# Performance work log

Measured on AMD Instinct MI355X. Metric: run time of the kernel, lower is better.

Reference implementation:

```python
import jax, jax.numpy as jnp
import numpy as np

C = 64
D = C // 8  # Q/K channel dim
B, H, W = 4, 64, 64


def setup_inputs() -> dict:
    key = jax.random.key(0)
    ks = jax.random.split(key, 4)
    x = jax.random.normal(ks[0], (B, C, H, W), dtype=jnp.float32)
    # 1x1 conv weights collapse to matrices [out_ch, in_ch]
    Wq = jax.random.normal(ks[1], (D, C), dtype=jnp.float32) * (1.0 / np.sqrt(C))
    Wk = jax.random.normal(ks[2], (D, C), dtype=jnp.float32) * (1.0 / np.sqrt(C))
    Wv = jax.random.normal(ks[3], (C, C), dtype=jnp.float32) * (1.0 / np.sqrt(C))
    bq = jnp.zeros((D,), jnp.float32)
    bk = jnp.zeros((D,), jnp.float32)
    bv = jnp.zeros((C,), jnp.float32)
    gamma = jnp.zeros((1,), jnp.float32)  # initialized to zero as in the module
    return {"x": x, "Wq": Wq, "bq": bq, "Wk": Wk, "bk": bk,
            "Wv": Wv, "bv": bv, "gamma": gamma}


def reference(x, Wq, bq, Wk, bk, Wv, bv, gamma):
    b, c, h, w = x.shape
    n = h * w
    xf = x.reshape(b, c, n)  # [B, C, N]
    # 1x1 convs == per-pixel linear projections
    q = jnp.einsum('dc,bcn->bdn', Wq, xf) + bq[None, :, None]  # [B, D, N]
    k = jnp.einsum('dc,bcn->bdn', Wk, xf) + bk[None, :, None]  # [B, D, N]
    v = jnp.einsum('ec,bcn->ben', Wv, xf) + bv[None, :, None]  # [B, C, N]
    # energy[b, i, j] = sum_d q[b, d, i] * k[b, d, j]  (query index i, key index j)
    energy = jnp.einsum('bdi,bdj->bij', q, k)  # [B, N, N]
    attn = jax.nn.softmax(energy, axis=-1)     # [B, N, N]
    # out[b, c, i] = sum_j v[b, c, j] * attn[b, i, j]
    out = jnp.einsum('bcj,bij->bci', v, attn)  # [B, C, N]
    out = out.reshape(b, c, h, w)
    return gamma[0] * out + x
```

## Files before the change

### kernel.cpp

```cpp
#include <hip/hip_runtime.h>
#include <hip/hip_bf16.h>

#define NPIX 4096

typedef __attribute__((ext_vector_type(16))) float f32x16;
typedef __attribute__((ext_vector_type(8))) short short8;

__device__ inline short f2bf(float f) {
  unsigned u = __float_as_uint(f);
  u += 0x7FFF + ((u >> 16) & 1);
  return (short)(u >> 16);
}

__device__ inline void gload16(const short* g, short* l) {
  __builtin_amdgcn_global_load_lds(
      (const __attribute__((address_space(1))) void*)g,
      (__attribute__((address_space(3))) void*)l, 16, 0, 0);
}

__global__ __launch_bounds__(256) void proj_kernel(
    const float* __restrict__ x,
    const float* __restrict__ Wq, const float* __restrict__ bq,
    const float* __restrict__ Wk, const float* __restrict__ bk,
    const float* __restrict__ Wv, const float* __restrict__ bv,
    short* __restrict__ Qp, short* __restrict__ Kp, short* __restrict__ Vi)
{
  const int job = blockIdx.x >> 6;
  const int p = (blockIdx.x & 63) * 256 + threadIdx.x;
  const int b = p >> 12, n = p & 4095;
  const float* xb = x + ((size_t)b << 18) + n;

  float xv[64];
#pragma unroll
  for (int c = 0; c < 64; ++c) xv[c] = xb[(size_t)c << 12];

  if (job < 2) {
    const float* W    = job ? Wk : Wq;
    const float* bias = job ? bk : bq;
    float a[8];
#pragma unroll
    for (int d = 0; d < 8; ++d) {
      float acc = bias[d];
#pragma unroll
      for (int c = 0; c < 64; ++c) acc = fmaf(W[d * 64 + c], xv[c], acc);
      a[d] = acc;
    }
    short8 o;
    if (job == 0) {
#pragma unroll
      for (int d = 0; d < 8; ++d) o[d] = f2bf(a[d] * 1.44269504f);
      *(short8*)(Qp + (size_t)p * 8) = o;
    } else {
#pragma unroll
      for (int d = 0; d < 8; ++d) o[d] = f2bf(a[d]);
      *(short8*)(Kp + (size_t)p * 8) = o;
    }
  } else {
    const int e0 = (job - 2) * 8;
    const size_t base = ((size_t)(b * 512 + (n >> 3)) * 64) * 8 + (n & 7);
#pragma unroll
    for (int i = 0; i < 8; ++i) {
      float acc = bv[e0 + i];
#pragma unroll
      for (int c = 0; c < 64; ++c) acc = fmaf(Wv[(e0 + i) * 64 + c], xv[c], acc);
      Vi[base + (size_t)(e0 + i) * 8] = f2bf(acc);
    }
  }
}

__device__ inline void pk_swap(const float* p, short8& A0, short8& A1) {
  unsigned u[8];
#pragma unroll
  for (int j = 0; j < 8; ++j)
    asm("v_cvt_pk_bf16_f32 %0, %1, %2" : "=v"(u[j]) : "v"(p[2 * j]), "v"(p[2 * j + 1]));
  asm("v_permlane32_swap_b32 %0, %1" : "+v"(u[0]), "+v"(u[2]));
  asm("v_permlane32_swap_b32 %0, %1" : "+v"(u[1]), "+v"(u[3]));
  asm("v_permlane32_swap_b32 %0, %1" : "+v"(u[4]), "+v"(u[6]));
  asm("v_permlane32_swap_b32 %0, %1" : "+v"(u[5]), "+v"(u[7]));
  union { unsigned w[4]; short8 s; } c0, c1;
  c0.w[0] = u[0]; c0.w[1] = u[1]; c0.w[2] = u[2]; c0.w[3] = u[3];
  c1.w[0] = u[4]; c1.w[1] = u[5]; c1.w[2] = u[6]; c1.w[3] = u[7];
  A0 = c0.s; A1 = c1.s;
}

__global__ __launch_bounds__(512, 2) void attn_kernel(
    const short* __restrict__ Qp, const short* __restrict__ Kp,
    const short* __restrict__ Vi,
    short* __restrict__ accB, float* __restrict__ psumW)
{
  __shared__ short kLds[2][1024];
  __shared__ short vLds[2][8192];

  const int tid  = threadIdx.x;
  const int wv   = tid >> 6;
  const int lane = tid & 63;
  const int lo   = lane & 31;
  const int hi   = lane >> 5;

  const int bid = blockIdx.x;
  const int ks  = bid & 3;
  const int qg  = (bid >> 2) & 15;
  const int b   = bid >> 6;
  const int Qgbase = (b << 12) + qg * 256 + wv * 32;

  short8 qf = {};
  if (hi == 0) qf = *(const short8*)(Qp + (size_t)(Qgbase + lo) * 8);

  const short* ksrc = Kp + ((size_t)(b << 12) + ks * 1024) * 8;
  const short* vsrc = Vi + (size_t)b * 262144 + (size_t)ks * 65536;

  auto stage = [&](int c, int buf) {
    const short* vs = vsrc + (size_t)c * 8192;
    gload16(vs + (size_t)tid * 8,         &vLds[buf][(tid & ~63) * 8]);
    gload16(vs + (size_t)(tid + 512) * 8, &vLds[buf][((tid + 512) & ~63) * 8]);
    if (tid < 128)
      gload16(ksrc + (size_t)c * 1024 + (size_t)tid * 8, &kLds[buf][(tid & ~63) * 8]);
  };

  f32x16 acc0 = {}, acc1 = {};
  float psum = 0.f;
  const f32x16 z = {};

  stage(0, 0);
  __syncthreads();

  for (int c = 0; c < 8; ++c) {
    if (c < 7) stage(c + 1, (c + 1) & 1);
    const int buf = c & 1;
#pragma unroll
    for (int i = 0; i < 4; ++i) {
      short8 kf = *(const short8*)&kLds[buf][(i * 32 + lo) * 8];
      f32x16 en = __builtin_amdgcn_mfma_f32_32x32x16_bf16(kf, qf, z, 0, 0, 0);
      float p[16];
#pragma unroll
      for (int j = 0; j < 16; ++j) p[j] = __builtin_amdgcn_exp2f(en[j]);
#pragma unroll
      for (int j = 0; j < 16; ++j) psum += p[j];
      short8 a0, a1;
      pk_swap(p, a0, a1);
      short8 v00 = *(const short8*)&vLds[buf][(i * 4 + hi) * 512 + lo * 8];
      short8 v01 = *(const short8*)&vLds[buf][(i * 4 + hi) * 512 + (32 + lo) * 8];
      short8 v10 = *(const short8*)&vLds[buf][(i * 4 + 2 + hi) * 512 + lo * 8];
      short8 v11 = *(const short8*)&vLds[buf][(i * 4 + 2 + hi) * 512 + (32 + lo) * 8];
      __builtin_amdgcn_s_setprio(1);
      acc0 = __builtin_amdgcn_mfma_f32_32x32x16_bf16(a0, v00, acc0, 0, 0, 0);
      acc1 = __builtin_amdgcn_mfma_f32_32x32x16_bf16(a0, v01, acc1, 0, 0, 0);
      acc0 = __builtin_amdgcn_mfma_f32_32x32x16_bf16(a1, v10, acc0, 0, 0, 0);
      acc1 = __builtin_amdgcn_mfma_f32_32x32x16_bf16(a1, v11, acc1, 0, 0, 0);
      __builtin_amdgcn_s_setprio(0);
    }
    __syncthreads();
  }

  float pfull = psum + __shfl_xor(psum, 32);
  if (hi == 0) psumW[ks * 16384 + Qgbase + lo] = pfull;

#pragma unroll
  for (int r = 0; r < 16; ++r) {
    const int q = (r & 3) + 8 * (r >> 2) + 4 * hi;
    const size_t base = ((size_t)(ks * 16384 + Qgbase + q)) << 6;
    accB[base + lo]      = f2bf(acc0[r]);
    accB[base + 32 + lo] = f2bf(acc1[r]);
  }
}

__global__ __launch_bounds__(256) void reduce_kernel(
    const short* __restrict__ accB, const float* __restrict__ psumW,
    const float* __restrict__ x, const float* __restrict__ gamma,
    float* __restrict__ out)
{
  __shared__ float accLds[64][65];
  __shared__ float sInv[64];

  const int tid = threadIdx.x;
  const int Qg0 = blockIdx.x * 64;
  const float g = gamma[0];

  if (tid < 64) {
    float s = 0.f;
#pragma unroll
    for (int ks = 0; ks < 4; ++ks) s += psumW[ks * 16384 + Qg0 + tid];
    sInv[tid] = g / s;
  }

  const int e2 = tid & 31;
  const int qr = tid >> 5;
#pragma unroll
  for (int qs = 0; qs < 8; ++qs) {
    const int qq = qr + qs * 8;
    float s0 = 0.f, s1 = 0.f;
#pragma unroll
    for (int ks = 0; ks < 4; ++ks) {
      const unsigned u = *(const unsigned*)&accB[(((size_t)(ks * 16384 + Qg0 + qq)) << 6) + e2 * 2];
      s0 += __uint_as_float(u << 16);
      s1 += __uint_as_float(u & 0xFFFF0000u);
    }
    accLds[qq][e2 * 2]     = s0;
    accLds[qq][e2 * 2 + 1] = s1;
  }
  __syncthreads();

  const int q  = tid & 63;
  const int er = tid >> 6;
  const int b  = (Qg0 + q) >> 12;
  const int n  = (Qg0 + q) & 4095;
  const float si = sInv[q];
#pragma unroll
  for (int k = 0; k < 16; ++k) {
    const int e = er + k * 4;
    const size_t idx = ((size_t)(b * 64 + e) << 12) + n;
    out[idx] = fmaf(si, accLds[q][e], x[idx]);
  }
}

extern "C" void kernel_launch(void* const* d_in, const int* in_sizes, int n_in,
                              void* d_out, int out_size, void* d_ws, size_t ws_size,
                              hipStream_t stream) {
  const float* x     = (const float*)d_in[0];
  const float* Wq    = (const float*)d_in[1];
  const float* bq    = (const float*)d_in[2];
  const float* Wk    = (const float*)d_in[3];
  const float* bk    = (const float*)d_in[4];
  const float* Wv    = (const float*)d_in[5];
  const float* bv    = (const float*)d_in[6];
  const float* gamma = (const float*)d_in[7];
  float* out = (float*)d_out;

  short* ws   = (short*)d_ws;
  short* Qp   = ws;
  short* Kp   = ws + 131072;
  short* Vi   = ws + 262144;
  short* accB = ws + 1310720;
  float* psumW = (float*)(ws + 5505024);

  proj_kernel<<<640, 256, 0, stream>>>(x, Wq, bq, Wk, bk, Wv, bv, Qp, Kp, Vi);
  attn_kernel<<<256, 512, 0, stream>>>(Qp, Kp, Vi, accB, psumW);
  reduce_kernel<<<256, 256, 0, stream>>>(accB, psumW, x, gamma, out);
}
```

Measured before the change: 104.9 us.

## Reuse K/V tiles across two query blocks per wave and split keys within block

Each wave in the attention kernel now handles 64 queries (two 32-query MFMA tiles) that share each loaded K and V fragment. Pairs of waves split the key range, so the block stages two key halves at once and writes eight partial slots instead of four. The reduce kernel is widened to sum the eight slots. The projection kernel is regrouped so one job computes both Q and K, and the V jobs compute 32 channels each, which cuts redundant x loads. In exchange, register pressure rises, LDS use doubles, and the workspace traffic for partial accumulators doubles.

New measurement: 132.1 us. 1.26x slower.

```diff
diff --git a/kernel.cpp b/kernel.cpp
--- a/kernel.cpp
+++ b/kernel.cpp
@@ -18,15 +18,15 @@
       (__attribute__((address_space(3))) void*)l, 16, 0, 0);
 }
 
-__global__ __launch_bounds__(256) void proj_kernel(
+__global__ __launch_bounds__(128) void proj_kernel(
     const float* __restrict__ x,
     const float* __restrict__ Wq, const float* __restrict__ bq,
     const float* __restrict__ Wk, const float* __restrict__ bk,
     const float* __restrict__ Wv, const float* __restrict__ bv,
     short* __restrict__ Qp, short* __restrict__ Kp, short* __restrict__ Vi)
 {
-  const int job = blockIdx.x >> 6;
-  const int p = (blockIdx.x & 63) * 256 + threadIdx.x;
+  const int job = blockIdx.x >> 7;
+  const int p = (blockIdx.x & 127) * 128 + threadIdx.x;
   const int b = p >> 12, n = p & 4095;
   const float* xb = x + ((size_t)b << 18) + n;
 
@@ -34,37 +34,39 @@
 #pragma unroll
   for (int c = 0; c < 64; ++c) xv[c] = xb[(size_t)c << 12];
 
-  if (job < 2) {
-    const float* W    = job ? Wk : Wq;
-    const float* bias = job ? bk : bq;
-    float a[8];
+  if (job == 0) {
+    float qa[8], ka[8];
 #pragma unroll
     for (int d = 0; d < 8; ++d) {
-      float acc = bias[d];
-#pragma unroll
-      for (int c = 0; c < 64; ++c) acc = fmaf(W[d * 64 + c], xv[c], acc);
-      a[d] = acc;
-    }
-    short8 o;
-    if (job == 0) {
-#pragma unroll
-      for (int d = 0; d < 8; ++d) o[d] = f2bf(a[d] * 1.44269504f);
-      *(short8*)(Qp + (size_t)p * 8) = o;
-    } else {
-#pragma unroll
-      for (int d = 0; d < 8; ++d) o[d] = f2bf(a[d]);
-      *(short8*)(Kp + (size_t)p * 8) = o;
-    }
+      float aq = bq[d], ak = bk[d];
+#pragma unroll
+      for (int c = 0; c < 64; ++c) {
+        aq = fmaf(Wq[d * 64 + c], xv[c], aq);
+        ak = fmaf(Wk[d * 64 + c], xv[c], ak);
+      }
+      qa[d] = aq; ka[d] = ak;
+    }
+    short8 qo, ko;
+#pragma unroll
+    for (int d = 0; d < 8; ++d) {
+      qo[d] = f2bf(qa[d] * 1.44269504f);
+      ko[d] = f2bf(ka[d]);
+    }
+    *(short8*)(Qp + (size_t)p * 8) = qo;
+    *(short8*)(Kp + (size_t)p * 8) = ko;
   } else {
-    const int e0 = (job - 2) * 8;
+    const int e0 = (job - 1) * 32;
+    float a[32];
+#pragma unroll
+    for (int i = 0; i < 32; ++i) {
+      float acc = bv[e0 + i];
+#pragma unroll
+      for (int c = 0; c < 64; ++c) acc = fmaf(Wv[(e0 + i) * 64 + c], xv[c], acc);
+      a[i] = acc;
+    }
     const size_t base = ((size_t)(b * 512 + (n >> 3)) * 64) * 8 + (n & 7);
 #pragma unroll
-    for (int i = 0; i < 8; ++i) {
-      float acc = bv[e0 + i];
-#pragma unroll
-      for (int c = 0; c < 64; ++c) acc = fmaf(Wv[(e0 + i) * 64 + c], xv[c], acc);
-      Vi[base + (size_t)(e0 + i) * 8] = f2bf(acc);
-    }
+    for (int i = 0; i < 32; ++i) Vi[base + (size_t)(e0 + i) * 8] = f2bf(a[i]);
   }
 }
 
@@ -83,16 +85,18 @@
   A0 = c0.s; A1 = c1.s;
 }
 
-__global__ __launch_bounds__(512, 2) void attn_kernel(
+__global__ __launch_bounds__(512) void attn_kernel(
     const short* __restrict__ Qp, const short* __restrict__ Kp,
     const short* __restrict__ Vi,
     short* __restrict__ accB, float* __restrict__ psumW)
 {
-  __shared__ short kLds[2][1024];
-  __shared__ short vLds[2][8192];
+  __shared__ short kLds[2][2][1024];
+  __shared__ short vLds[2][2][8192];
 
   const int tid  = threadIdx.x;
   const int wv   = tid >> 6;
+  const int qs   = wv >> 1;
+  const int ks2  = wv & 1;
   const int lane = tid & 63;
   const int lo   = lane & 31;
   const int hi   = lane >> 5;
@@ -101,66 +105,100 @@
   const int ks  = bid & 3;
   const int qg  = (bid >> 2) & 15;
   const int b   = bid >> 6;
-  const int Qgbase = (b << 12) + qg * 256 + wv * 32;
-
-  short8 qf = {};
-  if (hi == 0) qf = *(const short8*)(Qp + (size_t)(Qgbase + lo) * 8);
+  const int Qt  = (b << 12) + qg * 256 + qs * 64;
+  const int slot = ks * 2 + ks2;
+
+  short8 qf0 = {}, qf1 = {};
+  if (hi == 0) {
+    qf0 = *(const short8*)(Qp + (size_t)(Qt + lo) * 8);
+    qf1 = *(const short8*)(Qp + (size_t)(Qt + 32 + lo) * 8);
+  }
 
   const short* ksrc = Kp + ((size_t)(b << 12) + ks * 1024) * 8;
   const short* vsrc = Vi + (size_t)b * 262144 + (size_t)ks * 65536;
 
-  auto stage = [&](int c, int buf) {
-    const short* vs = vsrc + (size_t)c * 8192;
-    gload16(vs + (size_t)tid * 8,         &vLds[buf][(tid & ~63) * 8]);
-    gload16(vs + (size_t)(tid + 512) * 8, &vLds[buf][((tid + 512) & ~63) * 8]);
-    if (tid < 128)
-      gload16(ksrc + (size_t)c * 1024 + (size_t)tid * 8, &kLds[buf][(tid & ~63) * 8]);
+  auto stage = [&](int s, int buf) {
+#pragma unroll
+    for (int h = 0; h < 2; ++h) {
+      const short* vs = vsrc + (size_t)(h * 4 + s) * 8192;
+      gload16(vs + (size_t)tid * 8,         &vLds[buf][h][(tid & ~63) * 8]);
+      gload16(vs + (size_t)(tid + 512) * 8, &vLds[buf][h][((tid + 512) & ~63) * 8]);
+    }
+    if (tid < 256) {
+      const int h = tid >> 7, t = tid & 127;
+      gload16(ksrc + (size_t)(h * 4 + s) * 1024 + (size_t)t * 8,
+              &kLds[buf][h][(t & ~63) * 8]);
+    }
   };
 
-  f32x16 acc0 = {}, acc1 = {};
-  float psum = 0.f;
+  f32x16 acc00 = {}, acc01 = {}, acc10 = {}, acc11 = {};
+  float psum0 = 0.f, psum1 = 0.f;
   const f32x16 z = {};
 
   stage(0, 0);
   __syncthreads();
 
-  for (int c = 0; c < 8; ++c) {
-    if (c < 7) stage(c + 1, (c + 1) & 1);
-    const int buf = c & 1;
+  for (int s = 0; s < 4; ++s) {
+    if (s < 3) stage(s + 1, (s + 1) & 1);
+    const int buf = s & 1;
+    const short* kbuf = &kLds[buf][ks2][0];
+    const short* vbuf = &vLds[buf][ks2][0];
 #pragma unroll
     for (int i = 0; i < 4; ++i) {
-      short8 kf = *(const short8*)&kLds[buf][(i * 32 + lo) * 8];
-      f32x16 en = __builtin_amdgcn_mfma_f32_32x32x16_bf16(kf, qf, z, 0, 0, 0);
+      short8 kf = *(const short8*)&kbuf[(i * 32 + lo) * 8];
+      short8 v00 = *(const short8*)&vbuf[(i * 4 + hi) * 512 + lo * 8];
+      short8 v01 = *(const short8*)&vbuf[(i * 4 + hi) * 512 + (32 + lo) * 8];
+      short8 v10 = *(const short8*)&vbuf[(i * 4 + 2 + hi) * 512 + lo * 8];
+      short8 v11 = *(const short8*)&vbuf[(i * 4 + 2 + hi) * 512 + (32 + lo) * 8];
+
+      f32x16 en = __builtin_amdgcn_mfma_f32_32x32x16_bf16(kf, qf0, z, 0, 0, 0);
       float p[16];
 #pragma unroll
       for (int j = 0; j < 16; ++j) p[j] = __builtin_amdgcn_exp2f(en[j]);
 #pragma unroll
-      for (int j = 0; j < 16; ++j) psum += p[j];
+      for (int j = 0; j < 16; ++j) psum0 += p[j];
       short8 a0, a1;
       pk_swap(p, a0, a1);
-      short8 v00 = *(const short8*)&vLds[buf][(i * 4 + hi) * 512 + lo * 8];
-      short8 v01 = *(const short8*)&vLds[buf][(i * 4 + hi) * 512 + (32 + lo) * 8];
-      short8 v10 = *(const short8*)&vLds[buf][(i * 4 + 2 + hi) * 512 + lo * 8];
-      short8 v11 = *(const short8*)&vLds[buf][(i * 4 + 2 + hi) * 512 + (32 + lo) * 8];
       __builtin_amdgcn_s_setprio(1);
-      acc0 = __builtin_amdgcn_mfma_f32_32x32x16_bf16(a0, v00, acc0, 0, 0, 0);
-      acc1 = __builtin_amdgcn_mfma_f32_32x32x16_bf16(a0, v01, acc1, 0, 0, 0);
-      acc0 = __builtin_amdgcn_mfma_f32_32x32x16_bf16(a1, v10, acc0, 0, 0, 0);
-      acc1 = __builtin_amdgcn_mfma_f32_32x32x16_bf16(a1, v11, acc1, 0, 0, 0);
+      acc00 = __builtin_amdgcn_mfma_f32_32x32x16_bf16(a0, v00, acc00, 0, 0, 0);
+      acc01 = __builtin_amdgcn_mfma_f32_32x32x16_bf16(a0, v01, acc01, 0, 0, 0);
+      acc00 = __builtin_amdgcn_mfma_f32_32x32x16_bf16(a1, v10, acc00, 0, 0, 0);
+      acc01 = __builtin_amdgcn_mfma_f32_32x32x16_bf16(a1, v11, acc01, 0, 0, 0);
       __builtin_amdgcn_s_setprio(0);
+
+      en = __builtin_amdgcn_mfma_f32_32x32x16_bf16(kf, qf1, z, 0, 0, 0);
+#pragma unroll
+      for (int j = 0; j < 16; ++j) p[j] = __builtin_amdgcn_exp2f(en[j]);
+#pragma unroll
+      for (int j = 0; j < 16; ++j) psum1 += p[j];
+      short8 b0, b1;
+      pk_swap(p, b0, b1);
+      __builtin_amdgcn_s_setprio(1);
+      acc10 = __builtin_amdgcn_mfma_f32_32x32x16_bf16(b0, v00, acc10, 0, 0, 0);
+      acc11 = __builtin_amdgcn_mfma_f32_32x32x16_bf16(b0, v01, acc11, 0, 0, 0);
+      acc10 = __builtin_amdgcn_mfma_f32_32x32x16_bf16(b1, v10, acc10, 0, 0, 0);
+      acc11 = __builtin_amdgcn_mfma_f32_32x32x16_bf16(b1, v11, acc11, 0, 0, 0);
+      __builtin_amdgcn_s_setprio(0);
     }
     __syncthreads();
   }
 
-  float pfull = psum + __shfl_xor(psum, 32);
-  if (hi == 0) psumW[ks * 16384 + Qgbase + lo] = pfull;
+  float pf0 = psum0 + __shfl_xor(psum0, 32);
+  float pf1 = psum1 + __shfl_xor(psum1, 32);
+  if (hi == 0) {
+    psumW[slot * 16384 + Qt + lo]      = pf0;
+    psumW[slot * 16384 + Qt + 32 + lo] = pf1;
+  }
 
 #pragma unroll
   for (int r = 0; r < 16; ++r) {
     const int q = (r & 3) + 8 * (r >> 2) + 4 * hi;
-    const size_t base = ((size_t)(ks * 16384 + Qgbase + q)) << 6;
-    accB[base + lo]      = f2bf(acc0[r]);
-    accB[base + 32 + lo] = f2bf(acc1[r]);
+    const size_t b0i = ((size_t)(slot * 16384 + Qt + q)) << 6;
+    const size_t b1i = ((size_t)(slot * 16384 + Qt + 32 + q)) << 6;
+    accB[b0i + lo]      = f2bf(acc00[r]);
+    accB[b0i + 32 + lo] = f2bf(acc01[r]);
+    accB[b1i + lo]      = f2bf(acc10[r]);
+    accB[b1i + 32 + lo] = f2bf(acc11[r]);
   }
 }
 
@@ -179,19 +217,19 @@
   if (tid < 64) {
     float s = 0.f;
 #pragma unroll
-    for (int ks = 0; ks < 4; ++ks) s += psumW[ks * 16384 + Qg0 + tid];
+    for (int sl = 0; sl < 8; ++sl) s += psumW[sl * 16384 + Qg0 + tid];
     sInv[tid] = g / s;
   }
 
   const int e2 = tid & 31;
   const int qr = tid >> 5;
 #pragma unroll
-  for (int qs = 0; qs < 8; ++qs) {
-    const int qq = qr + qs * 8;
+  for (int qsw = 0; qsw < 8; ++qsw) {
+    const int qq = qr + qsw * 8;
     float s0 = 0.f, s1 = 0.f;
 #pragma unroll
-    for (int ks = 0; ks < 4; ++ks) {
-      const unsigned u = *(const unsigned*)&accB[(((size_t)(ks * 16384 + Qg0 + qq)) << 6) + e2 * 2];
+    for (int sl = 0; sl < 8; ++sl) {
+      const unsigned u = *(const unsigned*)&accB[(((size_t)(sl * 16384 + Qg0 + qq)) << 6) + e2 * 2];
       s0 += __uint_as_float(u << 16);
       s1 += __uint_as_float(u & 0xFFFF0000u);
     }
@@ -226,14 +264,14 @@
   const float* gamma = (const float*)d_in[7];
   float* out = (float*)d_out;
 
-  short* ws   = (short*)d_ws;
-  short* Qp   = ws;
-  short* Kp   = ws + 131072;
-  short* Vi   = ws + 262144;
-  short* accB = ws + 1310720;
-  float* psumW = (float*)(ws + 5505024);
-
-  proj_kernel<<<640, 256, 0, stream>>>(x, Wq, bq, Wk, bk, Wv, bv, Qp, Kp, Vi);
+  short* ws    = (short*)d_ws;
+  short* Qp    = ws;
+  short* Kp    = ws + 131072;
+  short* Vi    = ws + 262144;
+  short* accB  = ws + 1310720;
+  float* psumW = (float*)(ws + 9699328);
+
+  proj_kernel<<<384, 128, 0, stream>>>(x, Wq, bq, Wk, bk, Wv, bv, Qp, Kp, Vi);
   attn_kernel<<<256, 512, 0, stream>>>(Qp, Kp, Vi, accB, psumW);
   reduce_kernel<<<256, 256, 0, stream>>>(accB, psumW, x, gamma, out);
 }
```
